# Optimization experiments

Measured on AMD Instinct MI355X. Metric: run time of the kernel, lower is better.

Reference implementation:

```python
import jax, jax.numpy as jnp
import numpy as np

COMMITMENT_COST = 0.25
EPS = 1e-12  # matches torch F.normalize default eps


def _l2norm(v, axis=-1):
    n = jnp.linalg.norm(v, axis=axis, keepdims=True)
    return v / jnp.maximum(n, EPS)


def setup_inputs() -> dict:
    key = jax.random.key(0)
    k1, k2 = jax.random.split(key)
    x = jax.random.normal(k1, (65536, 256), dtype=jnp.float32)
    codebook = jax.random.normal(k2, (4096, 256), dtype=jnp.float32)
    return {"x": x, "codebook": codebook}


def reference(x, codebook):
    # x: [N, D] latents; codebook: [K, D] embedding table
    xn = _l2norm(x)                 # [N, D]
    cbn = _l2norm(codebook)         # [K, D]

    # Squared L2 distances: ||xn||^2 + ||cbn||^2 - 2 xn.cbn^T  -> [N, K]
    dists = (
        jnp.sum(xn * xn, axis=-1, keepdims=True)
        + jnp.sum(cbn * cbn, axis=1)
        - 2.0 * jnp.einsum("nd,kd->nk", xn, cbn)
    )
    idx = jnp.argmin(dists, axis=1)  # [N]

    # quantize: gather then L2-normalize (matches F.normalize(embeddings(idx)))
    quantized = _l2norm(cbn[idx])    # [N, D]

    q_latent_loss = jnp.mean((quantized - jax.lax.stop_gradient(xn)) ** 2)
    e_latent_loss = jnp.mean((xn - jax.lax.stop_gradient(quantized)) ** 2)
    loss = q_latent_loss + COMMITMENT_COST * e_latent_loss

    # straight-through estimator
    quantized_st = xn + jax.lax.stop_gradient(quantized - xn)
    return quantized_st, loss, idx
```

## Files before the change

### kernel.cpp

```cpp
#include <hip/hip_runtime.h>
#include <math.h>

#define N_ROWS 65536
#define DIM    256
#define NCODE  4096
#define MARGIN 2e-4f
#define TILE_C 32
#define NTILE  (NCODE / TILE_C)
#define FB     8
#define KCH    1024
#define NCH    (NCODE / KCH)
#define FIXG   512

typedef __attribute__((ext_vector_type(8)))  short short8v;
typedef __attribute__((ext_vector_type(4)))  float float4v;
typedef __attribute__((ext_vector_type(16))) float f32x16;

__device__ inline unsigned short f2bf(float f) {
    unsigned u = __float_as_uint(f);
    unsigned r = (u + 0x7fffu + ((u >> 16) & 1u)) >> 16;
    return (unsigned short)r;
}
__device__ inline float bf2f(unsigned short h) {
    return __uint_as_float(((unsigned)h) << 16);
}
__device__ inline void gll16(const void* g, void* l) {
    __builtin_amdgcn_global_load_lds(
        (const __attribute__((address_space(1))) unsigned int*)g,
        (__attribute__((address_space(3))) unsigned int*)l, 16, 0, 0);
}

__global__ void prep_kernel(const float* __restrict__ cb,
                            const float* __restrict__ x,
                            unsigned short* __restrict__ pk,
                            float* __restrict__ c2,
                            double* __restrict__ c2d,
                            double* __restrict__ ndi,
                            float* __restrict__ nx,
                            float* __restrict__ scx,
                            int* __restrict__ counter) {
    int t = threadIdx.x;
    if (blockIdx.x < NCODE) {
        int k = blockIdx.x;
        float v = cb[k * DIM + t];
        double dv = (double)v;
        double ss = dv * dv;
        __shared__ double red2[4], red3[4], redn[4];
        #pragma unroll
        for (int off = 32; off > 0; off >>= 1) ss += __shfl_down(ss, off);
        if ((t & 63) == 0) redn[t >> 6] = ss;
        __syncthreads();
        double S = redn[0] + redn[1] + redn[2] + redn[3];
        double nrm = fmax(sqrt(S), 1e-12);
        double cq = dv / nrm;
        float cf = (float)cq;
        unsigned short hb = f2bf(cf);
        unsigned short lb = f2bf(cf - bf2f(hb));
        {
            int cb32 = k >> 5, klo = k & 31, ks = t >> 4, hi = (t >> 3) & 1, j = t & 7;
            size_t ch = ((size_t)cb32 * 16 + ks) * 2;
            size_t slot = (size_t)(hi * 32 + klo) * 8 + j;
            pk[(ch + 0) * 512 + slot] = hb;
            pk[(ch + 1) * 512 + slot] = lb;
        }
        double s2 = (double)cf * (double)cf;
        double s3 = cq * cq;
        #pragma unroll
        for (int off = 32; off > 0; off >>= 1) {
            s2 += __shfl_down(s2, off);
            s3 += __shfl_down(s3, off);
        }
        if ((t & 63) == 0) { red2[t >> 6] = s2; red3[t >> 6] = s3; }
        __syncthreads();
        if (t == 0) {
            c2[k]  = (float)(red2[0] + red2[1] + red2[2] + red2[3]);
            c2d[k] = red3[0] + red3[1] + red3[2] + red3[3];
            ndi[k] = 1.0 / nrm;
        }
    } else {
        int xb = blockIdx.x - NCODE;
        if (xb == 0 && t == 0) counter[0] = 0;
        int w = t >> 6;
        int lane = t & 63;
        int row = xb * 4 + w;
        float4 v = ((const float4*)(x + (size_t)row * DIM))[lane];
        double ss = (double)v.x * v.x + (double)v.y * v.y
                  + (double)v.z * v.z + (double)v.w * v.w;
        #pragma unroll
        for (int off = 32; off > 0; off >>= 1) ss += __shfl_down(ss, off);
        if (lane == 0) {
            double n = fmax(sqrt(ss), 1e-12);
            nx[row]  = (float)n;
            scx[row] = (float)(2.0 / n);
        }
    }
}

__attribute__((amdgpu_waves_per_eu(2, 2)))
__global__ void __launch_bounds__(256)
argmin_mfma_kernel(const float* __restrict__ x,
                   const unsigned short* __restrict__ pk,
                   const float* __restrict__ c2,
                   const float* __restrict__ scx,
                   int* __restrict__ idx_out,
                   int* __restrict__ counter,
                   int* __restrict__ rowlist) {
    __shared__ unsigned short buf[2][16384];
    __shared__ float c2s[NCODE];

    int tid  = threadIdx.x;
    int lane = tid & 63;
    int wave = tid >> 6;
    int cl31 = lane & 31;
    int hi   = lane >> 5;
    int xbase = blockIdx.x * 128 + wave * 32;

    #pragma unroll
    for (int i = 0; i < NCODE / 256; i++) c2s[i * 256 + tid] = c2[i * 256 + tid];

    short8v bh[16], bl[16];
    const float* xr = x + (size_t)(xbase + cl31) * DIM + hi * 8;
    #pragma unroll
    for (int ks = 0; ks < 16; ks++) {
        float4 f0 = *(const float4*)(xr + ks * 16);
        float4 f1 = *(const float4*)(xr + ks * 16 + 4);
        float e[8] = {f0.x, f0.y, f0.z, f0.w, f1.x, f1.y, f1.z, f1.w};
        short8v h, l;
        #pragma unroll
        for (int j = 0; j < 8; j++) {
            unsigned short hb = f2bf(e[j]);
            h[j] = (short)hb;
            l[j] = (short)f2bf(e[j] - bf2f(hb));
        }
        bh[ks] = h;
        bl[ks] = l;
    }
    float scr = scx[xbase + cl31];

    float s1 = 3.4e38f, s2 = 3.4e38f;
    int   i1 = 0x7fffffff;

    {
        const unsigned short* src = pk + ((size_t)wave * 8) * 512 + lane * 8;
        unsigned short* dst = &buf[0][(wave * 8) * 512];
        #pragma unroll
        for (int i = 0; i < 8; i++) gll16(src + i * 512, dst + i * 512);
    }
    __syncthreads();

    int cur = 0;
    for (int t = 0; t < NTILE; t++) {
        int cbb = t * TILE_C;

        if (t + 1 < NTILE) {
            const unsigned short* src =
                pk + ((size_t)(t + 1) * 32 + wave * 8) * 512 + lane * 8;
            unsigned short* dst = &buf[cur ^ 1][(wave * 8) * 512];
            #pragma unroll
            for (int i = 0; i < 8; i++) gll16(src + i * 512, dst + i * 512);
        }

        const unsigned short* cbuf = &buf[cur][0];
        f32x16 a1 = {0.f,0.f,0.f,0.f,0.f,0.f,0.f,0.f,0.f,0.f,0.f,0.f,0.f,0.f,0.f,0.f};
        f32x16 a2 = a1, a3 = a1;
        #pragma unroll
        for (int ks = 0; ks < 16; ks++) {
            short8v ah = *(const short8v*)(cbuf + (size_t)(ks * 2 + 0) * 512 + lane * 8);
            short8v al = *(const short8v*)(cbuf + (size_t)(ks * 2 + 1) * 512 + lane * 8);
            a1 = __builtin_amdgcn_mfma_f32_32x32x16_bf16(ah, bh[ks], a1, 0, 0, 0);
            a2 = __builtin_amdgcn_mfma_f32_32x32x16_bf16(ah, bl[ks], a2, 0, 0, 0);
            a3 = __builtin_amdgcn_mfma_f32_32x32x16_bf16(al, bh[ks], a3, 0, 0, 0);
        }

        float4v gq0 = *(const float4v*)&c2s[cbb + hi * 4];
        float4v gq1 = *(const float4v*)&c2s[cbb + hi * 4 + 8];
        float4v gq2 = *(const float4v*)&c2s[cbb + hi * 4 + 16];
        float4v gq3 = *(const float4v*)&c2s[cbb + hi * 4 + 24];
        float sv[16];
        float mn = 3.4e38f;
        #pragma unroll
        for (int g = 0; g < 4; g++) {
            float4v gg = (g == 0) ? gq0 : (g == 1) ? gq1 : (g == 2) ? gq2 : gq3;
            #pragma unroll
            for (int q = 0; q < 4; q++) {
                int r = g * 4 + q;
                float s = gg[q] - scr * (a1[r] + a2[r] + a3[r]);
                sv[r] = s;
                mn = fminf(mn, s);
            }
        }
        if (!__all(mn >= s2)) {
            #pragma unroll
            for (int g = 0; g < 4; g++) {
                #pragma unroll
                for (int q = 0; q < 4; q++) {
                    float s = sv[g * 4 + q];
                    int ci = cbb + q + 8 * g + 4 * hi;
                    if (s < s1) { s2 = s1; s1 = s; i1 = ci; }
                    else if (s < s2) s2 = s;
                }
            }
        }

        __syncthreads();
        cur ^= 1;
    }

    {
        float o1 = __shfl_xor(s1, 32);
        int   oi = __shfl_xor(i1, 32);
        float o2 = __shfl_xor(s2, 32);
        if (o1 < s1 || (o1 == s1 && oi < i1)) { s2 = fminf(s1, o2); s1 = o1; i1 = oi; }
        else                                   { s2 = fminf(o1, s2); }
    }
    if (lane < 32) {
        int row = xbase + lane;
        idx_out[row] = i1;
        if (s2 - s1 < MARGIN) { int slot = atomicAdd(counter, 1); rowlist[slot] = row; }
    }
}

__global__ void fixup2d_kernel(const float* __restrict__ x,
                               const float* __restrict__ cb,
                               const double* __restrict__ c2d,
                               const double* __restrict__ ndi,
                               const int* __restrict__ counter,
                               const int* __restrict__ rowlist,
                               double* __restrict__ pb_s,
                               int* __restrict__ pb_i) {
    __shared__ double xs[FB][DIM];
    __shared__ double isx_sh[FB];
    __shared__ double red_s[4][FB];
    __shared__ int    red_i[4][FB];
    int t = threadIdx.x, lane = t & 63, wave = t >> 6;
    int cnt = counter[0];
    int nbat = (cnt + FB - 1) / FB;
    int nwork = nbat * NCH;

    for (int w = blockIdx.x; w < nwork; w += FIXG) {
        int batch = w / NCH, chunk = w - batch * NCH;
        int base = batch * FB;
        int nb = cnt - base; if (nb > FB) nb = FB;

        #pragma unroll
        for (int r = 0; r < FB; r++)
            if (r < nb) xs[r][t] = (double)x[(size_t)rowlist[base + r] * DIM + t];
        __syncthreads();

        for (int rr = wave; rr < nb; rr += 4) {
            double a0 = xs[rr][lane],       a1 = xs[rr][lane + 64];
            double a2 = xs[rr][lane + 128], a3 = xs[rr][lane + 192];
            double ss = a0 * a0 + a1 * a1 + a2 * a2 + a3 * a3;
            #pragma unroll
            for (int m = 1; m < 64; m <<= 1) ss += __shfl_xor(ss, m);
            if (lane == 0) isx_sh[rr] = 2.0 / fmax(sqrt(ss), 1e-12);
        }
        __syncthreads();

        double bs[FB]; int bi[FB];
        #pragma unroll
        for (int r = 0; r < FB; r++) { bs[r] = 1e300; bi[r] = 0x7fffffff; }

        for (int k0 = 0; k0 < KCH / 256; k0++) {
            int k = chunk * KCH + k0 * 256 + t;
            const float4* cr = (const float4*)(cb + (size_t)k * DIM);
            double d[FB];
            #pragma unroll
            for (int r = 0; r < FB; r++) d[r] = 0.0;
            #pragma unroll 4
            for (int d4 = 0; d4 < DIM / 4; d4++) {
                float4 c = cr[d4];
                double cx = c.x, cy = c.y, cz = c.z, cw = c.w;
                int dd = d4 * 4;
                #pragma unroll
                for (int r = 0; r < FB; r++) {
                    d[r] = fma(cx, xs[r][dd],     d[r]);
                    d[r] = fma(cy, xs[r][dd + 1], d[r]);
                    d[r] = fma(cz, xs[r][dd + 2], d[r]);
                    d[r] = fma(cw, xs[r][dd + 3], d[r]);
                }
            }
            double ndik = ndi[k], c2k = c2d[k];
            #pragma unroll
            for (int r = 0; r < FB; r++) {
                double sc = c2k - isx_sh[r] * d[r] * ndik;
                if (sc < bs[r] || (sc == bs[r] && k < bi[r])) { bs[r] = sc; bi[r] = k; }
            }
        }

        #pragma unroll
        for (int r = 0; r < FB; r++) {
            double b = bs[r]; int idx = bi[r];
            #pragma unroll
            for (int m = 1; m < 64; m <<= 1) {
                double ob = __shfl_xor(b, m);
                int   oi = __shfl_xor(idx, m);
                if (ob < b || (ob == b && oi < idx)) { b = ob; idx = oi; }
            }
            if (lane == 0) { red_s[wave][r] = b; red_i[wave][r] = idx; }
        }
        __syncthreads();
        if (t < nb) {
            double b = red_s[0][t]; int idx = red_i[0][t];
            #pragma unroll
            for (int ww = 1; ww < 4; ww++) {
                double ob = red_s[ww][t]; int oi = red_i[ww][t];
                if (ob < b || (ob == b && oi < idx)) { b = ob; idx = oi; }
            }
            pb_s[(size_t)(base + t) * NCH + chunk] = b;
            pb_i[(size_t)(base + t) * NCH + chunk] = idx;
        }
        __syncthreads();
    }
}

__global__ void fixmerge_kernel(const int* __restrict__ counter,
                                const int* __restrict__ rowlist,
                                const double* __restrict__ pb_s,
                                const int* __restrict__ pb_i,
                                int* __restrict__ idxv) {
    int cnt = counter[0];
    for (int s = blockIdx.x * 256 + threadIdx.x; s < cnt; s += gridDim.x * 256) {
        double b = pb_s[(size_t)s * NCH]; int idx = pb_i[(size_t)s * NCH];
        #pragma unroll
        for (int c = 1; c < NCH; c++) {
            double ob = pb_s[(size_t)s * NCH + c]; int oi = pb_i[(size_t)s * NCH + c];
            if (ob < b || (ob == b && oi < idx)) { b = ob; idx = oi; }
        }
        idxv[rowlist[s]] = idx;
    }
}

__global__ void gather_loss_kernel(const float* __restrict__ x,
                                   const float* __restrict__ cb,
                                   const double* __restrict__ ndi,
                                   const float* __restrict__ nx,
                                   const int* __restrict__ idxv,
                                   float* __restrict__ out_q,
                                   float* __restrict__ out_idxf,
                                   float* __restrict__ partials) {
    int w = threadIdx.x >> 6, lane = threadIdx.x & 63;
    int row = blockIdx.x * 4 + w;
    int iv = idxv[row];
    float ndif = (float)ndi[iv];
    float inx = 1.0f / nx[row];
    float4 q4 = ((const float4*)(cb + (size_t)iv * DIM))[lane];
    float4 x4 = ((const float4*)(x + (size_t)row * DIM))[lane];
    float4 qq;
    qq.x = q4.x * ndif; qq.y = q4.y * ndif;
    qq.z = q4.z * ndif; qq.w = q4.w * ndif;
    ((float4*)(out_q + (size_t)row * DIM))[lane] = qq;
    float dx = qq.x - x4.x * inx;
    float dy = qq.y - x4.y * inx;
    float dz = qq.z - x4.z * inx;
    float dw = qq.w - x4.w * inx;
    float ss = dx * dx + dy * dy + dz * dz + dw * dw;
    #pragma unroll
    for (int off = 32; off > 0; off >>= 1) ss += __shfl_down(ss, off);
    if (lane == 0) {
        partials[row] = ss;
        out_idxf[row] = (float)iv;
    }
}

__global__ void loss_reduce_kernel(const float* __restrict__ partials,
                                   float* __restrict__ out_loss) {
    int t = threadIdx.x;
    float s = 0.0f;
    for (int i = t; i < N_ROWS; i += 256) s += partials[i];
    __shared__ float red[4];
    #pragma unroll
    for (int off = 32; off > 0; off >>= 1) s += __shfl_down(s, off);
    if ((t & 63) == 0) red[t >> 6] = s;
    __syncthreads();
    if (t == 0) out_loss[0] = 1.25f * (red[0] + red[1] + red[2] + red[3]) / (float)(N_ROWS * DIM);
}

extern "C" void kernel_launch(void* const* d_in, const int* in_sizes, int n_in,
                              void* d_out, int out_size, void* d_ws, size_t ws_size,
                              hipStream_t stream) {
    const float* x  = (const float*)d_in[0];
    const float* cb = (const float*)d_in[1];
    float* out = (float*)d_out;

    double* c2d  = (double*)d_ws;
    double* ndi  = c2d + NCODE;
    double* pb_s = ndi + NCODE;
    float*  c2   = (float*)(pb_s + (size_t)N_ROWS * NCH);
    float*  nx   = c2 + NCODE;
    float*  scx  = nx + N_ROWS;
    int*    idxv = (int*)(scx + N_ROWS);
    float*  partials = (float*)(idxv + N_ROWS);
    int*    counter  = (int*)(partials + N_ROWS);
    int*    rowlist  = counter + 8;
    int*    pb_i     = rowlist + N_ROWS;
    unsigned short* pk = (unsigned short*)(pb_i + (size_t)N_ROWS * NCH);

    float* out_q    = out;
    float* out_loss = out + (size_t)N_ROWS * DIM;
    float* out_idxf = out_loss + 1;

    hipLaunchKernelGGL(prep_kernel, dim3(NCODE + N_ROWS / 4), dim3(256), 0, stream,
                       cb, x, pk, c2, c2d, ndi, nx, scx, counter);
    hipLaunchKernelGGL(argmin_mfma_kernel, dim3(N_ROWS / 128), dim3(256), 0, stream,
                       x, pk, c2, scx, idxv, counter, rowlist);
    hipLaunchKernelGGL(fixup2d_kernel, dim3(FIXG), dim3(256), 0, stream,
                       x, cb, c2d, ndi, counter, rowlist, pb_s, pb_i);
    hipLaunchKernelGGL(fixmerge_kernel, dim3(64), dim3(256), 0, stream,
                       counter, rowlist, pb_s, pb_i, idxv);
    hipLaunchKernelGGL(gather_loss_kernel, dim3(N_ROWS / 4), dim3(256), 0, stream,
                       x, cb, ndi, nx, idxv, out_q, out_idxf, partials);
    hipLaunchKernelGGL(loss_reduce_kernel, dim3(1), dim3(256), 0, stream,
                       partials, out_loss);
}
```

Measured before the change: 599.1 us.

## Fuse fixup merge into gather kernel via per-row slot map

```diff
diff --git a/kernel.cpp b/kernel.cpp
--- a/kernel.cpp
+++ b/kernel.cpp
@@ -38,7 +38,8 @@
                             double* __restrict__ ndi,
                             float* __restrict__ nx,
                             float* __restrict__ scx,
-                            int* __restrict__ counter) {
+                            int* __restrict__ counter,
+                            int* __restrict__ fslot) {
     int t = threadIdx.x;
     if (blockIdx.x < NCODE) {
         int k = blockIdx.x;
@@ -82,16 +83,20 @@
         if (xb == 0 && t == 0) counter[0] = 0;
         int w = t >> 6;
         int lane = t & 63;
-        int row = xb * 4 + w;
-        float4 v = ((const float4*)(x + (size_t)row * DIM))[lane];
-        double ss = (double)v.x * v.x + (double)v.y * v.y
-                  + (double)v.z * v.z + (double)v.w * v.w;
-        #pragma unroll
-        for (int off = 32; off > 0; off >>= 1) ss += __shfl_down(ss, off);
-        if (lane == 0) {
-            double n = fmax(sqrt(ss), 1e-12);
-            nx[row]  = (float)n;
-            scx[row] = (float)(2.0 / n);
+        if (t < 16) fslot[xb * 16 + t] = 0;
+        #pragma unroll
+        for (int r = 0; r < 4; r++) {
+            int row = xb * 16 + w * 4 + r;
+            float4 v = ((const float4*)(x + (size_t)row * DIM))[lane];
+            double ss = (double)v.x * v.x + (double)v.y * v.y
+                      + (double)v.z * v.z + (double)v.w * v.w;
+            #pragma unroll
+            for (int off = 32; off > 0; off >>= 1) ss += __shfl_down(ss, off);
+            if (lane == 0) {
+                double n = fmax(sqrt(ss), 1e-12);
+                nx[row]  = (float)n;
+                scx[row] = (float)(2.0 / n);
+            }
         }
     }
 }
@@ -104,7 +109,8 @@
                    const float* __restrict__ scx,
                    int* __restrict__ idx_out,
                    int* __restrict__ counter,
-                   int* __restrict__ rowlist) {
+                   int* __restrict__ rowlist,
+                   int* __restrict__ fslot) {
     __shared__ unsigned short buf[2][16384];
     __shared__ float c2s[NCODE];
 
@@ -216,7 +222,11 @@
     if (lane < 32) {
         int row = xbase + lane;
         idx_out[row] = i1;
-        if (s2 - s1 < MARGIN) { int slot = atomicAdd(counter, 1); rowlist[slot] = row; }
+        if (s2 - s1 < MARGIN) {
+            int slot = atomicAdd(counter, 1);
+            rowlist[slot] = row;
+            fslot[row] = slot + 1;
+        }
     }
 }
 
@@ -314,34 +324,32 @@
     }
 }
 
-__global__ void fixmerge_kernel(const int* __restrict__ counter,
-                                const int* __restrict__ rowlist,
-                                const double* __restrict__ pb_s,
-                                const int* __restrict__ pb_i,
-                                int* __restrict__ idxv) {
-    int cnt = counter[0];
-    for (int s = blockIdx.x * 256 + threadIdx.x; s < cnt; s += gridDim.x * 256) {
-        double b = pb_s[(size_t)s * NCH]; int idx = pb_i[(size_t)s * NCH];
-        #pragma unroll
-        for (int c = 1; c < NCH; c++) {
-            double ob = pb_s[(size_t)s * NCH + c]; int oi = pb_i[(size_t)s * NCH + c];
-            if (ob < b || (ob == b && oi < idx)) { b = ob; idx = oi; }
-        }
-        idxv[rowlist[s]] = idx;
-    }
-}
-
 __global__ void gather_loss_kernel(const float* __restrict__ x,
                                    const float* __restrict__ cb,
                                    const double* __restrict__ ndi,
                                    const float* __restrict__ nx,
                                    const int* __restrict__ idxv,
+                                   const int* __restrict__ fslot,
+                                   const double* __restrict__ pb_s,
+                                   const int* __restrict__ pb_i,
                                    float* __restrict__ out_q,
                                    float* __restrict__ out_idxf,
                                    float* __restrict__ partials) {
     int w = threadIdx.x >> 6, lane = threadIdx.x & 63;
     int row = blockIdx.x * 4 + w;
-    int iv = idxv[row];
+    int fs = fslot[row];
+    int iv;
+    if (fs > 0) {
+        int s = fs - 1;
+        double b = pb_s[(size_t)s * NCH]; iv = pb_i[(size_t)s * NCH];
+        #pragma unroll
+        for (int c = 1; c < NCH; c++) {
+            double ob = pb_s[(size_t)s * NCH + c]; int oi = pb_i[(size_t)s * NCH + c];
+            if (ob < b || (ob == b && oi < iv)) { b = ob; iv = oi; }
+        }
+    } else {
+        iv = idxv[row];
+    }
     float ndif = (float)ndi[iv];
     float inx = 1.0f / nx[row];
     float4 q4 = ((const float4*)(cb + (size_t)iv * DIM))[lane];
@@ -367,7 +375,11 @@
                                    float* __restrict__ out_loss) {
     int t = threadIdx.x;
     float s = 0.0f;
-    for (int i = t; i < N_ROWS; i += 256) s += partials[i];
+    const float4* p4 = (const float4*)partials;
+    for (int i = t; i < N_ROWS / 4; i += 256) {
+        float4 v = p4[i];
+        s += v.x + v.y + v.z + v.w;
+    }
     __shared__ float red[4];
     #pragma unroll
     for (int off = 32; off > 0; off >>= 1) s += __shfl_down(s, off);
@@ -393,23 +405,22 @@
     float*  partials = (float*)(idxv + N_ROWS);
     int*    counter  = (int*)(partials + N_ROWS);
     int*    rowlist  = counter + 8;
-    int*    pb_i     = rowlist + N_ROWS;
+    int*    fslot    = rowlist + N_ROWS;
+    int*    pb_i     = fslot + N_ROWS;
     unsigned short* pk = (unsigned short*)(pb_i + (size_t)N_ROWS * NCH);
 
     float* out_q    = out;
     float* out_loss = out + (size_t)N_ROWS * DIM;
     float* out_idxf = out_loss + 1;
 
-    hipLaunchKernelGGL(prep_kernel, dim3(NCODE + N_ROWS / 4), dim3(256), 0, stream,
-                       cb, x, pk, c2, c2d, ndi, nx, scx, counter);
+    hipLaunchKernelGGL(prep_kernel, dim3(NCODE + N_ROWS / 16), dim3(256), 0, stream,
+                       cb, x, pk, c2, c2d, ndi, nx, scx, counter, fslot);
     hipLaunchKernelGGL(argmin_mfma_kernel, dim3(N_ROWS / 128), dim3(256), 0, stream,
-                       x, pk, c2, scx, idxv, counter, rowlist);
+                       x, pk, c2, scx, idxv, counter, rowlist, fslot);
     hipLaunchKernelGGL(fixup2d_kernel, dim3(FIXG), dim3(256), 0, stream,
                        x, cb, c2d, ndi, counter, rowlist, pb_s, pb_i);
-    hipLaunchKernelGGL(fixmerge_kernel, dim3(64), dim3(256), 0, stream,
-                       counter, rowlist, pb_s, pb_i, idxv);
     hipLaunchKernelGGL(gather_loss_kernel, dim3(N_ROWS / 4), dim3(256), 0, stream,
-                       x, cb, ndi, nx, idxv, out_q, out_idxf, partials);
+                       x, cb, ndi, nx, idxv, fslot, pb_s, pb_i, out_q, out_idxf, partials);
     hipLaunchKernelGGL(loss_reduce_kernel, dim3(1), dim3(256), 0, stream,
                        partials, out_loss);
 }
```

New measurement: 554.5 us. 7.4% less time.
